# Performance work log

Hardware: AMD Instinct MI355X
Metric: run time of the kernel (lower is better)

## Reference

```python
import jax, jax.numpy as jnp
import numpy as np

D = 768
H = 12
DH = D // H


def setup_inputs() -> dict:
    key = jax.random.key(0)
    ks = jax.random.split(key, 7)
    B, S = 8, 1024
    sequences = jax.random.normal(ks[0], (B, S, D), dtype=jnp.float32)
    # per-head Linear params: weight [H, DH, DH] (torch Linear convention y = x W^T + b), bias [H, DH]
    scale = 1.0 / np.sqrt(DH)
    Wq = jax.random.uniform(ks[1], (H, DH, DH), jnp.float32, -scale, scale)
    Wk = jax.random.uniform(ks[2], (H, DH, DH), jnp.float32, -scale, scale)
    Wv = jax.random.uniform(ks[3], (H, DH, DH), jnp.float32, -scale, scale)
    bq = jax.random.uniform(ks[4], (H, DH), jnp.float32, -scale, scale)
    bk = jax.random.uniform(ks[5], (H, DH), jnp.float32, -scale, scale)
    bv = jax.random.uniform(ks[6], (H, DH), jnp.float32, -scale, scale)
    return {"sequences": sequences, "Wq": Wq, "Wk": Wk, "Wv": Wv,
            "bq": bq, "bk": bk, "bv": bv}


def reference(sequences, Wq, Wk, Wv, bq, bk, bv):
    B, S, _ = sequences.shape
    x = sequences.reshape(B, S, H, DH)  # head slices along feature dim
    # torch Linear: y = x @ W.T + b  ->  einsum over last dim of W
    Q = jnp.einsum('bshd,hed->bshe', x, Wq) + bq
    K = jnp.einsum('bshd,hed->bshe', x, Wk) + bk
    V = jnp.einsum('bshd,hed->bshe', x, Wv) + bv
    scores = jnp.einsum('bshe,bthe->bhst', Q, K) / np.sqrt(DH).astype(np.float32)
    attn = jax.nn.softmax(scores, axis=-1)  # [B,H,S,S]
    out = jnp.einsum('bhst,bthd->bshd', attn, V)
    return out.reshape(B, S, H * DH)
```

## Files before the change

### kernel.cpp

```cpp
#include <hip/hip_runtime.h>

#define NH 12
#define DHEAD 64
#define DMODEL 768
#define SEQ 1024
#define NBH 96

typedef _Float16 h8 __attribute__((ext_vector_type(8)));
typedef _Float16 h4 __attribute__((ext_vector_type(4)));
typedef __fp16   fp16x2 __attribute__((ext_vector_type(2)));
typedef float f32x4 __attribute__((ext_vector_type(4)));


__global__ __launch_bounds__(256) void proj_kernel(
    const float* __restrict__ x,
    const float* __restrict__ Wq, const float* __restrict__ Wk,
    const float* __restrict__ Wv,
    const float* __restrict__ bq, const float* __restrict__ bk,
    const float* __restrict__ bv,
    _Float16* __restrict__ Qf, _Float16* __restrict__ Kf,
    _Float16* __restrict__ Vf)
{
    __shared__ _Float16 xh[128][72];
    __shared__ _Float16 yh[128][72];

    const int h    = blockIdx.y;
    const int tid  = threadIdx.x;
    const int row0 = blockIdx.x * 128;
    const int lane = tid & 63;
    const int w    = tid >> 6;
    const int g    = lane >> 4;
    const int r    = lane & 15;

    const int b    = row0 >> 10;
    const int bh   = b * NH + h;
    const int s16b = (row0 & 1023) >> 4;
    const int s32b = (row0 & 1023) >> 5;

#pragma unroll
    for (int p = 0; p < 8; ++p) {
        const int rr = p * 16 + (tid >> 4);
        const int c4 = (tid & 15) * 4;
        float4 v = *(const float4*)(x + (size_t)(row0 + rr) * DMODEL
                                      + h * DHEAD + c4);
        h4 o = { (_Float16)v.x, (_Float16)v.y, (_Float16)v.z, (_Float16)v.w };
        *(h4*)(&xh[rr][c4]) = o;
    }
    __syncthreads();

#pragma unroll
    for (int mtx = 0; mtx < 3; ++mtx) {
        const float* W    = (mtx == 0 ? Wq : (mtx == 1 ? Wk : Wv)) + h * DHEAD * DHEAD;
        const float* bias = (mtx == 0 ? bq : (mtx == 1 ? bk : bv)) + h * DHEAD;
        const float  ws   = (mtx == 0) ? 0.125f * 1.44269504f : 1.0f;

        h8 bf[4][2];
        float bcol[4];
#pragma unroll
        for (int n = 0; n < 4; ++n) {
            const float* Wr = W + (n * 16 + r) * DHEAD;
#pragma unroll
            for (int hf = 0; hf < 2; ++hf) {
                const float* p = Wr + hf * 32 + g * 8;
                float4 w0 = *(const float4*)(p);
                float4 w1 = *(const float4*)(p + 4);
                h8 o = { (_Float16)(w0.x * ws), (_Float16)(w0.y * ws),
                         (_Float16)(w0.z * ws), (_Float16)(w0.w * ws),
                         (_Float16)(w1.x * ws), (_Float16)(w1.y * ws),
                         (_Float16)(w1.z * ws), (_Float16)(w1.w * ws) };
                bf[n][hf] = o;
            }
            bcol[n] = bias[n * 16 + r] * ws;
        }

#pragma unroll
        for (int gg = 0; gg < 2; ++gg) {
            const int gi = w + gg * 4;
            const h8 af0 = *(const h8*)(&xh[gi * 16 + r][g * 8]);
            const h8 af1 = *(const h8*)(&xh[gi * 16 + r][32 + g * 8]);
#pragma unroll
            for (int n = 0; n < 4; ++n) {
                f32x4 d = { bcol[n], bcol[n], bcol[n], bcol[n] };
                d = __builtin_amdgcn_mfma_f32_16x16x32_f16(af0, bf[n][0], d, 0, 0, 0);
                d = __builtin_amdgcn_mfma_f32_16x16x32_f16(af1, bf[n][1], d, 0, 0, 0);
#pragma unroll
                for (int reg = 0; reg < 4; ++reg)
                    yh[gi * 16 + g * 4 + reg][n * 16 + r] = (_Float16)d[reg];
            }
        }
        __syncthreads();

        if (mtx < 2) {
            const int s16l = tid >> 5;
            const int lx   = tid & 31;
            h8* dstb = (h8*)(mtx == 0 ? Qf : Kf)
                     + ((size_t)(bh * 64 + s16b + s16l)) * 128;
#pragma unroll
            for (int hf = 0; hf < 2; ++hf)
#pragma unroll
                for (int li = 0; li < 2; ++li) {
                    const int ln  = lx + li * 32;
                    const int gg2 = ln >> 4, rr2 = ln & 15;
                    h8 v = *(const h8*)(&yh[s16l * 16 + rr2][hf * 32 + gg2 * 8]);
                    dstb[hf * 64 + ln] = v;
                }
        } else {
            const int s32l = tid >> 6;
            const int t    = (tid >> 4) & 3;
            const int li   = tid & 15;
            h8 wv[4];
#pragma unroll
            for (int k = 0; k < 4; ++k) {
                const int ln  = li * 4 + k;
                const int gg2 = ln >> 4, rr2 = ln & 15;
#pragma unroll
                for (int j = 0; j < 4; ++j) {
                    wv[k][j]     = yh[s32l * 32 +      gg2 * 4 + j][t * 16 + rr2];
                    wv[k][j + 4] = yh[s32l * 32 + 16 + gg2 * 4 + j][t * 16 + rr2];
                }
            }
            h8* dst = (h8*)Vf
                    + (((size_t)(bh * 32 + s32b + s32l)) * 4 + t) * 64 + li * 4;
#pragma unroll
            for (int k = 0; k < 4; ++k) dst[k] = wv[k];
        }
        if (mtx < 2) __syncthreads();
    }
}

__global__ __launch_bounds__(256) void attn_kernel(
    const _Float16* __restrict__ Qf, const _Float16* __restrict__ Kf,
    const _Float16* __restrict__ Vf, float* __restrict__ out)
{
    __shared__ f32x4 osum[4][8][64];
    __shared__ float lred[4][4][16];

    const int orig    = blockIdx.x;
    const int logical = (orig & 7) * 192 + (orig >> 3);
    const int bh      = logical >> 4;
    const int qblk    = logical & 15;
    const int lane = threadIdx.x & 63;
    const int w    = threadIdx.x >> 6;
    const int g    = lane >> 4;
    const int r    = lane & 15;
    const int q0   = qblk * 64;

    const h8* Qb = (const h8*)Qf + ((size_t)bh * 64 + qblk * 4) * 128;
    const h8* Kw = (const h8*)Kf + (size_t)bh * 64 * 128 + (size_t)w * 16 * 128;
    const h8* Vw = (const h8*)Vf + (size_t)bh * 32 * 256 + (size_t)w * 8 * 256;

    h8 qf[4][2];
#pragma unroll
    for (int qg = 0; qg < 4; ++qg) {
        qf[qg][0] = Qb[qg * 128 + lane];
        qf[qg][1] = Qb[qg * 128 + 64 + lane];
    }

    f32x4 ot[4][4] = {};
    float lsum[4] = {};

    h8 kb0[2][2], kb1[2][2], vb[4];
#pragma unroll
    for (int kk = 0; kk < 2; ++kk) {
        kb0[kk][0] = Kw[kk * 128 + lane];
        kb0[kk][1] = Kw[kk * 128 + 64 + lane];
    }

#define ATTN_ITER(i, KC, KN, PREF)                                            \
    {                                                                         \
        _Pragma("unroll")                                                     \
        for (int t = 0; t < 4; ++t) vb[t] = Vw[(i) * 256 + t * 64 + lane];    \
        if (PREF) {                                                           \
            _Pragma("unroll")                                                 \
            for (int kk = 0; kk < 2; ++kk) {                                  \
                KN[kk][0] = Kw[((i) * 2 + 2 + kk) * 128 + lane];              \
                KN[kk][1] = Kw[((i) * 2 + 2 + kk) * 128 + 64 + lane];         \
            }                                                                 \
        }                                                                     \
        _Pragma("unroll")                                                     \
        for (int qg = 0; qg < 4; ++qg) {                                      \
            f32x4 s0 = __builtin_amdgcn_mfma_f32_16x16x32_f16(                \
                KC[0][0], qf[qg][0], (f32x4){0.f, 0.f, 0.f, 0.f}, 0, 0, 0);   \
            s0 = __builtin_amdgcn_mfma_f32_16x16x32_f16(                      \
                KC[0][1], qf[qg][1], s0, 0, 0, 0);                            \
            f32x4 s1 = __builtin_amdgcn_mfma_f32_16x16x32_f16(                \
                KC[1][0], qf[qg][0], (f32x4){0.f, 0.f, 0.f, 0.f}, 0, 0, 0);   \
            s1 = __builtin_amdgcn_mfma_f32_16x16x32_f16(                      \
                KC[1][1], qf[qg][1], s1, 0, 0, 0);                            \
            float p0 = __builtin_amdgcn_exp2f(s0[0]);                         \
            float p1 = __builtin_amdgcn_exp2f(s0[1]);                         \
            float p2 = __builtin_amdgcn_exp2f(s0[2]);                         \
            float p3 = __builtin_amdgcn_exp2f(s0[3]);                         \
            float p4 = __builtin_amdgcn_exp2f(s1[0]);                         \
            float p5 = __builtin_amdgcn_exp2f(s1[1]);                         \
            float p6 = __builtin_amdgcn_exp2f(s1[2]);                         \
            float p7 = __builtin_amdgcn_exp2f(s1[3]);                         \
            lsum[qg] += ((p0 + p1) + (p2 + p3)) + ((p4 + p5) + (p6 + p7));    \
            union { fp16x2 v2[2]; h4 v4; } ua, ub;                            \
            ua.v2[0] = __builtin_amdgcn_cvt_pkrtz(p0, p1);                    \
            ua.v2[1] = __builtin_amdgcn_cvt_pkrtz(p2, p3);                    \
            ub.v2[0] = __builtin_amdgcn_cvt_pkrtz(p4, p5);                    \
            ub.v2[1] = __builtin_amdgcn_cvt_pkrtz(p6, p7);                    \
            _Pragma("unroll")                                                 \
            for (int t = 0; t < 4; ++t) {                                     \
                h4 lo = __builtin_shufflevector(vb[t], vb[t], 0, 1, 2, 3);    \
                h4 hi = __builtin_shufflevector(vb[t], vb[t], 4, 5, 6, 7);    \
                ot[qg][t] = __builtin_amdgcn_mfma_f32_16x16x16f16(            \
                    lo, ua.v4, ot[qg][t], 0, 0, 0);                           \
                ot[qg][t] = __builtin_amdgcn_mfma_f32_16x16x16f16(            \
                    hi, ub.v4, ot[qg][t], 0, 0, 0);                           \
            }                                                                 \
        }                                                                     \
    }

    ATTN_ITER(0, kb0, kb1, 1)
    ATTN_ITER(1, kb1, kb0, 1)
    ATTN_ITER(2, kb0, kb1, 1)
    ATTN_ITER(3, kb1, kb0, 1)
    ATTN_ITER(4, kb0, kb1, 1)
    ATTN_ITER(5, kb1, kb0, 1)
    ATTN_ITER(6, kb0, kb1, 1)
    ATTN_ITER(7, kb1, kb0, 0)
#undef ATTN_ITER

#pragma unroll
    for (int qg = 0; qg < 4; ++qg) {
        lsum[qg] += __shfl_xor(lsum[qg], 16);
        lsum[qg] += __shfl_xor(lsum[qg], 32);
    }
    if (g == 0) {
#pragma unroll
        for (int qg = 0; qg < 4; ++qg) lred[w][qg][r] = lsum[qg];
    }

    const int b = bh / NH, h = bh % NH;
    float* obase = out + ((size_t)b * SEQ + q0) * DMODEL + h * DHEAD;

#pragma unroll
    for (int ph = 0; ph < 2; ++ph) {
        __syncthreads();
#pragma unroll
        for (int qg = 0; qg < 2; ++qg)
#pragma unroll
            for (int t = 0; t < 4; ++t)
                osum[w][qg * 4 + t][lane] = ot[ph * 2 + qg][t];
        __syncthreads();
#pragma unroll
        for (int pp = 0; pp < 2; ++pp) {
            const int pi  = w * 2 + pp;
            const int qgl = pi >> 2;
            const int qg  = ph * 2 + qgl;
            const int t   = pi & 3;
            f32x4 o = osum[0][pi][lane] + osum[1][pi][lane]
                    + osum[2][pi][lane] + osum[3][pi][lane];
            const float tot = (lred[0][qg][r] + lred[1][qg][r])
                            + (lred[2][qg][r] + lred[3][qg][r]);
            const float inv = 1.0f / tot;
            float4 res = { o[0] * inv, o[1] * inv, o[2] * inv, o[3] * inv };
            *(float4*)(obase + (size_t)(qg * 16 + r) * DMODEL
                       + t * 16 + g * 4) = res;
        }
    }
}

extern "C" void kernel_launch(void* const* d_in, const int* in_sizes, int n_in,
                              void* d_out, int out_size, void* d_ws, size_t ws_size,
                              hipStream_t stream)
{
    const float* x  = (const float*)d_in[0];
    const float* Wq = (const float*)d_in[1];
    const float* Wk = (const float*)d_in[2];
    const float* Wv = (const float*)d_in[3];
    const float* bq = (const float*)d_in[4];
    const float* bk = (const float*)d_in[5];
    const float* bv = (const float*)d_in[6];
    float* out = (float*)d_out;

    const size_t frag_elems = (size_t)NBH * 64 * 2 * 64 * 8;
    _Float16* Qf = (_Float16*)d_ws;
    _Float16* Kf = Qf + frag_elems;
    _Float16* Vf = Kf + frag_elems;

    proj_kernel<<<dim3(64, 12), 256, 0, stream>>>(x, Wq, Wk, Wv, bq, bk, bv,
                                                  Qf, Kf, Vf);
    attn_kernel<<<1536, 256, 0, stream>>>(Qf, Kf, Vf, out);
}
```

Baseline: 67.53 us.

## Split attention query rows across 8 waves and halve projection tile size

The attention kernel now runs 512 threads per block: two groups of four waves each take half of the 64 query rows, while the four key-quarters are kept. This halves per-wave accumulator registers and raises the number of resident waves. It also raises MFMA wave priority inside the inner loop with s_setprio. The projection kernel processes 64 rows per block instead of 128, doubling its grid for better CU coverage, at the cost of loading weights twice as often.

```diff
diff --git a/kernel.cpp b/kernel.cpp
--- a/kernel.cpp
+++ b/kernel.cpp
@@ -21,12 +21,12 @@
     _Float16* __restrict__ Qf, _Float16* __restrict__ Kf,
     _Float16* __restrict__ Vf)
 {
-    __shared__ _Float16 xh[128][72];
-    __shared__ _Float16 yh[128][72];
+    __shared__ _Float16 xh[64][72];
+    __shared__ _Float16 yh[64][72];
 
     const int h    = blockIdx.y;
     const int tid  = threadIdx.x;
-    const int row0 = blockIdx.x * 128;
+    const int row0 = blockIdx.x * 64;
     const int lane = tid & 63;
     const int w    = tid >> 6;
     const int g    = lane >> 4;
@@ -38,7 +38,7 @@
     const int s32b = (row0 & 1023) >> 5;
 
 #pragma unroll
-    for (int p = 0; p < 8; ++p) {
+    for (int p = 0; p < 4; ++p) {
         const int rr = p * 16 + (tid >> 4);
         const int c4 = (tid & 15) * 4;
         float4 v = *(const float4*)(x + (size_t)(row0 + rr) * DMODEL
@@ -73,11 +73,9 @@
             bcol[n] = bias[n * 16 + r] * ws;
         }
 
-#pragma unroll
-        for (int gg = 0; gg < 2; ++gg) {
-            const int gi = w + gg * 4;
-            const h8 af0 = *(const h8*)(&xh[gi * 16 + r][g * 8]);
-            const h8 af1 = *(const h8*)(&xh[gi * 16 + r][32 + g * 8]);
+        {
+            const h8 af0 = *(const h8*)(&xh[w * 16 + r][g * 8]);
+            const h8 af1 = *(const h8*)(&xh[w * 16 + r][32 + g * 8]);
 #pragma unroll
             for (int n = 0; n < 4; ++n) {
                 f32x4 d = { bcol[n], bcol[n], bcol[n], bcol[n] };
@@ -85,33 +83,30 @@
                 d = __builtin_amdgcn_mfma_f32_16x16x32_f16(af1, bf[n][1], d, 0, 0, 0);
 #pragma unroll
                 for (int reg = 0; reg < 4; ++reg)
-                    yh[gi * 16 + g * 4 + reg][n * 16 + r] = (_Float16)d[reg];
+                    yh[w * 16 + g * 4 + reg][n * 16 + r] = (_Float16)d[reg];
             }
         }
         __syncthreads();
 
         if (mtx < 2) {
-            const int s16l = tid >> 5;
-            const int lx   = tid & 31;
+            const int s16l = tid >> 6;
+            const int ln   = tid & 63;
+            const int gg2 = ln >> 4, rr2 = ln & 15;
             h8* dstb = (h8*)(mtx == 0 ? Qf : Kf)
                      + ((size_t)(bh * 64 + s16b + s16l)) * 128;
 #pragma unroll
             for (int hf = 0; hf < 2; ++hf)
-#pragma unroll
-                for (int li = 0; li < 2; ++li) {
-                    const int ln  = lx + li * 32;
-                    const int gg2 = ln >> 4, rr2 = ln & 15;
-                    h8 v = *(const h8*)(&yh[s16l * 16 + rr2][hf * 32 + gg2 * 8]);
-                    dstb[hf * 64 + ln] = v;
-                }
+                dstb[hf * 64 + ln] =
+                    *(const h8*)(&yh[s16l * 16 + rr2][hf * 32 + gg2 * 8]);
         } else {
-            const int s32l = tid >> 6;
-            const int t    = (tid >> 4) & 3;
-            const int li   = tid & 15;
-            h8 wv[4];
-#pragma unroll
-            for (int k = 0; k < 4; ++k) {
-                const int ln  = li * 4 + k;
+            const int s32l = tid >> 7;
+            const int rem  = tid & 127;
+            const int t    = rem >> 5;
+            const int li   = rem & 31;
+            h8 wv[2];
+#pragma unroll
+            for (int k = 0; k < 2; ++k) {
+                const int ln  = li * 2 + k;
                 const int gg2 = ln >> 4, rr2 = ln & 15;
 #pragma unroll
                 for (int j = 0; j < 4; ++j) {
@@ -120,20 +115,20 @@
                 }
             }
             h8* dst = (h8*)Vf
-                    + (((size_t)(bh * 32 + s32b + s32l)) * 4 + t) * 64 + li * 4;
-#pragma unroll
-            for (int k = 0; k < 4; ++k) dst[k] = wv[k];
+                    + (((size_t)(bh * 32 + s32b + s32l)) * 4 + t) * 64 + li * 2;
+            dst[0] = wv[0];
+            dst[1] = wv[1];
         }
         if (mtx < 2) __syncthreads();
     }
 }
 
-__global__ __launch_bounds__(256) void attn_kernel(
+__global__ __launch_bounds__(512, 4) void attn_kernel(
     const _Float16* __restrict__ Qf, const _Float16* __restrict__ Kf,
     const _Float16* __restrict__ Vf, float* __restrict__ out)
 {
     __shared__ f32x4 osum[4][8][64];
-    __shared__ float lred[4][4][16];
+    __shared__ float lred[8][2][16];
 
     const int orig    = blockIdx.x;
     const int logical = (orig & 7) * 192 + (orig >> 3);
@@ -141,23 +136,25 @@
     const int qblk    = logical & 15;
     const int lane = threadIdx.x & 63;
     const int w    = threadIdx.x >> 6;
+    const int qh   = w >> 2;
+    const int kq   = w & 3;
     const int g    = lane >> 4;
     const int r    = lane & 15;
     const int q0   = qblk * 64;
 
-    const h8* Qb = (const h8*)Qf + ((size_t)bh * 64 + qblk * 4) * 128;
-    const h8* Kw = (const h8*)Kf + (size_t)bh * 64 * 128 + (size_t)w * 16 * 128;
-    const h8* Vw = (const h8*)Vf + (size_t)bh * 32 * 256 + (size_t)w * 8 * 256;
-
-    h8 qf[4][2];
-#pragma unroll
-    for (int qg = 0; qg < 4; ++qg) {
+    const h8* Qb = (const h8*)Qf + ((size_t)bh * 64 + qblk * 4 + qh * 2) * 128;
+    const h8* Kw = (const h8*)Kf + (size_t)bh * 64 * 128 + (size_t)kq * 16 * 128;
+    const h8* Vw = (const h8*)Vf + (size_t)bh * 32 * 256 + (size_t)kq * 8 * 256;
+
+    h8 qf[2][2];
+#pragma unroll
+    for (int qg = 0; qg < 2; ++qg) {
         qf[qg][0] = Qb[qg * 128 + lane];
         qf[qg][1] = Qb[qg * 128 + 64 + lane];
     }
 
-    f32x4 ot[4][4] = {};
-    float lsum[4] = {};
+    f32x4 ot[2][4] = {};
+    float lsum[2] = {};
 
     h8 kb0[2][2], kb1[2][2], vb[4];
 #pragma unroll
@@ -177,8 +174,9 @@
                 KN[kk][1] = Kw[((i) * 2 + 2 + kk) * 128 + 64 + lane];         \
             }                                                                 \
         }                                                                     \
+        __builtin_amdgcn_s_setprio(1);                                        \
         _Pragma("unroll")                                                     \
-        for (int qg = 0; qg < 4; ++qg) {                                      \
+        for (int qg = 0; qg < 2; ++qg) {                                      \
             f32x4 s0 = __builtin_amdgcn_mfma_f32_16x16x32_f16(                \
                 KC[0][0], qf[qg][0], (f32x4){0.f, 0.f, 0.f, 0.f}, 0, 0, 0);   \
             s0 = __builtin_amdgcn_mfma_f32_16x16x32_f16(                      \
@@ -211,6 +209,7 @@
                     hi, ub.v4, ot[qg][t], 0, 0, 0);                           \
             }                                                                 \
         }                                                                     \
+        __builtin_amdgcn_s_setprio(0);                                        \
     }
 
     ATTN_ITER(0, kb0, kb1, 1)
@@ -224,13 +223,13 @@
 #undef ATTN_ITER
 
 #pragma unroll
-    for (int qg = 0; qg < 4; ++qg) {
+    for (int qg = 0; qg < 2; ++qg) {
         lsum[qg] += __shfl_xor(lsum[qg], 16);
         lsum[qg] += __shfl_xor(lsum[qg], 32);
     }
     if (g == 0) {
 #pragma unroll
-        for (int qg = 0; qg < 4; ++qg) lred[w][qg][r] = lsum[qg];
+        for (int qg = 0; qg < 2; ++qg) lred[w][qg][r] = lsum[qg];
     }
 
     const int b = bh / NH, h = bh % NH;
@@ -239,26 +238,26 @@
 #pragma unroll
     for (int ph = 0; ph < 2; ++ph) {
         __syncthreads();
-#pragma unroll
-        for (int qg = 0; qg < 2; ++qg)
-#pragma unroll
-            for (int t = 0; t < 4; ++t)
-                osum[w][qg * 4 + t][lane] = ot[ph * 2 + qg][t];
+        if (qh == ph) {
+#pragma unroll
+            for (int qg = 0; qg < 2; ++qg)
+#pragma unroll
+                for (int t = 0; t < 4; ++t)
+                    osum[kq][qg * 4 + t][lane] = ot[qg][t];
+        }
         __syncthreads();
-#pragma unroll
-        for (int pp = 0; pp < 2; ++pp) {
-            const int pi  = w * 2 + pp;
-            const int qgl = pi >> 2;
-            const int qg  = ph * 2 + qgl;
-            const int t   = pi & 3;
+        {
+            const int pi  = w;
+            const int qgm = pi >> 2;
+            const int tm  = pi & 3;
             f32x4 o = osum[0][pi][lane] + osum[1][pi][lane]
                     + osum[2][pi][lane] + osum[3][pi][lane];
-            const float tot = (lred[0][qg][r] + lred[1][qg][r])
-                            + (lred[2][qg][r] + lred[3][qg][r]);
+            const float tot = (lred[ph * 4 + 0][qgm][r] + lred[ph * 4 + 1][qgm][r])
+                            + (lred[ph * 4 + 2][qgm][r] + lred[ph * 4 + 3][qgm][r]);
             const float inv = 1.0f / tot;
             float4 res = { o[0] * inv, o[1] * inv, o[2] * inv, o[3] * inv };
-            *(float4*)(obase + (size_t)(qg * 16 + r) * DMODEL
-                       + t * 16 + g * 4) = res;
+            *(float4*)(obase + (size_t)(ph * 32 + qgm * 16 + r) * DMODEL
+                       + tm * 16 + g * 4) = res;
         }
     }
 }
@@ -281,7 +280,7 @@
     _Float16* Kf = Qf + frag_elems;
     _Float16* Vf = Kf + frag_elems;
 
-    proj_kernel<<<dim3(64, 12), 256, 0, stream>>>(x, Wq, Wk, Wv, bq, bk, bv,
-                                                  Qf, Kf, Vf);
-    attn_kernel<<<1536, 256, 0, stream>>>(Qf, Kf, Vf, out);
+    proj_kernel<<<dim3(128, 12), 256, 0, stream>>>(x, Wq, Wk, Wv, bq, bk, bv,
+                                                   Qf, Kf, Vf);
+    attn_kernel<<<1536, 512, 0, stream>>>(Qf, Kf, Vf, out);
 }
```

Measured after the change: 84.16 us. 24.6% more time.

## Split attention block into 8 waves over query halves with V prefetch and setprio

Applied to the files above, without the earlier changes.

Doubles the attention block to 512 threads so each wave handles two query groups instead of four. The four K-slice waves are now replicated across two query halves. V fragments are double-buffered and prefetched alongside K, and the MFMA/exp section runs under raised wave priority. The aim is more waves in flight to hide memory latency and fewer registers per wave. In exchange, each K/V tile is loaded twice per block and the reduction epilogue changes.

```diff
diff --git a/kernel.cpp b/kernel.cpp
--- a/kernel.cpp
+++ b/kernel.cpp
@@ -128,12 +128,12 @@
     }
 }
 
-__global__ __launch_bounds__(256) void attn_kernel(
+__global__ __launch_bounds__(512, 4) void attn_kernel(
     const _Float16* __restrict__ Qf, const _Float16* __restrict__ Kf,
     const _Float16* __restrict__ Vf, float* __restrict__ out)
 {
     __shared__ f32x4 osum[4][8][64];
-    __shared__ float lred[4][4][16];
+    __shared__ float lred[8][2][16];
 
     const int orig    = blockIdx.x;
     const int logical = (orig & 7) * 192 + (orig >> 3);
@@ -141,44 +141,50 @@
     const int qblk    = logical & 15;
     const int lane = threadIdx.x & 63;
     const int w    = threadIdx.x >> 6;
+    const int qh   = w >> 2;
+    const int kq   = w & 3;
     const int g    = lane >> 4;
     const int r    = lane & 15;
     const int q0   = qblk * 64;
 
-    const h8* Qb = (const h8*)Qf + ((size_t)bh * 64 + qblk * 4) * 128;
-    const h8* Kw = (const h8*)Kf + (size_t)bh * 64 * 128 + (size_t)w * 16 * 128;
-    const h8* Vw = (const h8*)Vf + (size_t)bh * 32 * 256 + (size_t)w * 8 * 256;
-
-    h8 qf[4][2];
-#pragma unroll
-    for (int qg = 0; qg < 4; ++qg) {
+    const h8* Qb = (const h8*)Qf + ((size_t)bh * 64 + qblk * 4 + qh * 2) * 128;
+    const h8* Kw = (const h8*)Kf + (size_t)bh * 64 * 128 + (size_t)kq * 16 * 128;
+    const h8* Vw = (const h8*)Vf + (size_t)bh * 32 * 256 + (size_t)kq * 8 * 256;
+
+    h8 qf[2][2];
+#pragma unroll
+    for (int qg = 0; qg < 2; ++qg) {
         qf[qg][0] = Qb[qg * 128 + lane];
         qf[qg][1] = Qb[qg * 128 + 64 + lane];
     }
 
-    f32x4 ot[4][4] = {};
-    float lsum[4] = {};
-
-    h8 kb0[2][2], kb1[2][2], vb[4];
+    f32x4 ot[2][4] = {};
+    float lsum[2] = {};
+
+    h8 kA[2][2], kB[2][2], vA[4], vB[4];
 #pragma unroll
     for (int kk = 0; kk < 2; ++kk) {
-        kb0[kk][0] = Kw[kk * 128 + lane];
-        kb0[kk][1] = Kw[kk * 128 + 64 + lane];
-    }
-
-#define ATTN_ITER(i, KC, KN, PREF)                                            \
+        kA[kk][0] = Kw[kk * 128 + lane];
+        kA[kk][1] = Kw[kk * 128 + 64 + lane];
+    }
+#pragma unroll
+    for (int t = 0; t < 4; ++t) vA[t] = Vw[t * 64 + lane];
+
+#define ATTN_ITER(i, KC, VC, KN, VN, PREF)                                    \
     {                                                                         \
-        _Pragma("unroll")                                                     \
-        for (int t = 0; t < 4; ++t) vb[t] = Vw[(i) * 256 + t * 64 + lane];    \
         if (PREF) {                                                           \
             _Pragma("unroll")                                                 \
             for (int kk = 0; kk < 2; ++kk) {                                  \
                 KN[kk][0] = Kw[((i) * 2 + 2 + kk) * 128 + lane];              \
                 KN[kk][1] = Kw[((i) * 2 + 2 + kk) * 128 + 64 + lane];         \
             }                                                                 \
+            _Pragma("unroll")                                                 \
+            for (int t = 0; t < 4; ++t)                                       \
+                VN[t] = Vw[((i) + 1) * 256 + t * 64 + lane];                  \
         }                                                                     \
+        __builtin_amdgcn_s_setprio(1);                                        \
         _Pragma("unroll")                                                     \
-        for (int qg = 0; qg < 4; ++qg) {                                      \
+        for (int qg = 0; qg < 2; ++qg) {                                      \
             f32x4 s0 = __builtin_amdgcn_mfma_f32_16x16x32_f16(                \
                 KC[0][0], qf[qg][0], (f32x4){0.f, 0.f, 0.f, 0.f}, 0, 0, 0);   \
             s0 = __builtin_amdgcn_mfma_f32_16x16x32_f16(                      \
@@ -203,34 +209,35 @@
             ub.v2[1] = __builtin_amdgcn_cvt_pkrtz(p6, p7);                    \
             _Pragma("unroll")                                                 \
             for (int t = 0; t < 4; ++t) {                                     \
-                h4 lo = __builtin_shufflevector(vb[t], vb[t], 0, 1, 2, 3);    \
-                h4 hi = __builtin_shufflevector(vb[t], vb[t], 4, 5, 6, 7);    \
+                h4 lo = __builtin_shufflevector(VC[t], VC[t], 0, 1, 2, 3);    \
+                h4 hi = __builtin_shufflevector(VC[t], VC[t], 4, 5, 6, 7);    \
                 ot[qg][t] = __builtin_amdgcn_mfma_f32_16x16x16f16(            \
                     lo, ua.v4, ot[qg][t], 0, 0, 0);                           \
                 ot[qg][t] = __builtin_amdgcn_mfma_f32_16x16x16f16(            \
                     hi, ub.v4, ot[qg][t], 0, 0, 0);                           \
             }                                                                 \
         }                                                                     \
-    }
-
-    ATTN_ITER(0, kb0, kb1, 1)
-    ATTN_ITER(1, kb1, kb0, 1)
-    ATTN_ITER(2, kb0, kb1, 1)
-    ATTN_ITER(3, kb1, kb0, 1)
-    ATTN_ITER(4, kb0, kb1, 1)
-    ATTN_ITER(5, kb1, kb0, 1)
-    ATTN_ITER(6, kb0, kb1, 1)
-    ATTN_ITER(7, kb1, kb0, 0)
+        __builtin_amdgcn_s_setprio(0);                                        \
+    }
+
+    ATTN_ITER(0, kA, vA, kB, vB, 1)
+    ATTN_ITER(1, kB, vB, kA, vA, 1)
+    ATTN_ITER(2, kA, vA, kB, vB, 1)
+    ATTN_ITER(3, kB, vB, kA, vA, 1)
+    ATTN_ITER(4, kA, vA, kB, vB, 1)
+    ATTN_ITER(5, kB, vB, kA, vA, 1)
+    ATTN_ITER(6, kA, vA, kB, vB, 1)
+    ATTN_ITER(7, kB, vB, kA, vA, 0)
 #undef ATTN_ITER
 
 #pragma unroll
-    for (int qg = 0; qg < 4; ++qg) {
+    for (int qg = 0; qg < 2; ++qg) {
         lsum[qg] += __shfl_xor(lsum[qg], 16);
         lsum[qg] += __shfl_xor(lsum[qg], 32);
     }
     if (g == 0) {
 #pragma unroll
-        for (int qg = 0; qg < 4; ++qg) lred[w][qg][r] = lsum[qg];
+        for (int qg = 0; qg < 2; ++qg) lred[w][qg][r] = lsum[qg];
     }
 
     const int b = bh / NH, h = bh % NH;
@@ -239,26 +246,26 @@
 #pragma unroll
     for (int ph = 0; ph < 2; ++ph) {
         __syncthreads();
-#pragma unroll
-        for (int qg = 0; qg < 2; ++qg)
-#pragma unroll
-            for (int t = 0; t < 4; ++t)
-                osum[w][qg * 4 + t][lane] = ot[ph * 2 + qg][t];
+        if (qh == ph) {
+#pragma unroll
+            for (int qg = 0; qg < 2; ++qg)
+#pragma unroll
+                for (int t = 0; t < 4; ++t)
+                    osum[kq][qg * 4 + t][lane] = ot[qg][t];
+        }
         __syncthreads();
-#pragma unroll
-        for (int pp = 0; pp < 2; ++pp) {
-            const int pi  = w * 2 + pp;
-            const int qgl = pi >> 2;
-            const int qg  = ph * 2 + qgl;
-            const int t   = pi & 3;
+        {
+            const int pi  = w;
+            const int qgm = pi >> 2;
+            const int tm  = pi & 3;
             f32x4 o = osum[0][pi][lane] + osum[1][pi][lane]
                     + osum[2][pi][lane] + osum[3][pi][lane];
-            const float tot = (lred[0][qg][r] + lred[1][qg][r])
-                            + (lred[2][qg][r] + lred[3][qg][r]);
+            const float tot = (lred[ph * 4 + 0][qgm][r] + lred[ph * 4 + 1][qgm][r])
+                            + (lred[ph * 4 + 2][qgm][r] + lred[ph * 4 + 3][qgm][r]);
             const float inv = 1.0f / tot;
             float4 res = { o[0] * inv, o[1] * inv, o[2] * inv, o[3] * inv };
-            *(float4*)(obase + (size_t)(qg * 16 + r) * DMODEL
-                       + t * 16 + g * 4) = res;
+            *(float4*)(obase + (size_t)(ph * 32 + qgm * 16 + r) * DMODEL
+                       + tm * 16 + g * 4) = res;
         }
     }
 }
@@ -283,5 +290,5 @@
 
     proj_kernel<<<dim3(64, 12), 256, 0, stream>>>(x, Wq, Wk, Wv, bq, bk, bv,
                                                   Qf, Kf, Vf);
-    attn_kernel<<<1536, 256, 0, stream>>>(Qf, Kf, Vf, out);
+    attn_kernel<<<1536, 512, 0, stream>>>(Qf, Kf, Vf, out);
 }
```

After: 100.9 us. +49.4%, slower.
